# Kernel tuning notes

Hardware: AMD Instinct MI355X
Metric: run time of the kernel (lower is better)

The kernel has to match this reference:

```python
import jax, jax.numpy as jnp
import numpy as np

DIM = 256
HEADS = 8
WS = 16      # window size
WN = 16      # num windows (img 64x64)
KS = 3
B = 16
IMG = 64


def setup_inputs() -> dict:
    key = jax.random.key(0)
    ks = jax.random.split(key, 12)
    d = DIM
    hid = d // 16  # SE hidden (d >= 64)
    inp = {
        "x": jax.random.normal(ks[0], (B, d, IMG, IMG), dtype=jnp.float32),
        "conv_w": jax.random.normal(ks[1], (WN, d, d, KS, KS), dtype=jnp.float32) * 0.02,
        "wqkv": jax.random.normal(ks[2], (d, 3 * d), dtype=jnp.float32) * 0.02,
        "bqkv": jax.random.normal(ks[3], (3 * d,), dtype=jnp.float32) * 0.02,
        "wout": jax.random.normal(ks[4], (d, d), dtype=jnp.float32) * 0.02,
        "bout": jax.random.normal(ks[5], (d,), dtype=jnp.float32) * 0.02,
        "se_w1": jax.random.normal(ks[6], (WN, hid, d), dtype=jnp.float32) * 0.05,
        "se_b1": jax.random.normal(ks[7], (WN, hid), dtype=jnp.float32) * 0.02,
        "se_w2": jax.random.normal(ks[8], (WN, d, hid), dtype=jnp.float32) * 0.05,
        "se_b2": jax.random.normal(ks[9], (WN, d), dtype=jnp.float32) * 0.02,
        "ln_g": jnp.ones((d,), dtype=jnp.float32),
        "ln_b": jnp.zeros((d,), dtype=jnp.float32),
    }
    return inp


def reference(x, conv_w, wqkv, bqkv, wout, bout, se_w1, se_b1, se_w2, se_b2, ln_g, ln_b):
    Bn, C, H, W = x.shape
    hd = C // HEADS
    scale = hd ** (-0.5)

    # window partition: (WN, B, C, WS, WS), windows in (h_idx, w_idx) row-major order
    xw = x.reshape(Bn, C, H // WS, WS, W // WS, WS).transpose(2, 4, 0, 1, 3, 5)
    xw = xw.reshape(WN, Bn, C, WS, WS)

    # kernel tokens: per-layer weight.view(B, C, -1).permute(0,2,1), cat on axis 1
    last = C * KS * KS // Bn
    kt = conv_w.reshape(WN, Bn, C, last).transpose(1, 0, 3, 2).reshape(Bn, WN * last, C)

    # self-attention over kernel tokens (batch axis becomes dim C after reshape)
    qkv = kt @ wqkv + bqkv                                    # (B, WN*last, 3C)
    qkv = qkv.reshape(C, WN * KS * KS, 3, HEADS, hd).transpose(2, 0, 3, 1, 4)
    q, k, v = qkv[0] * scale, qkv[1], qkv[2]                  # (C, H, T, hd), T = WN*KS*KS
    attn = jax.nn.softmax(jnp.einsum('dhqe,dhke->dhqk', q, k), axis=-1)
    o = jnp.einsum('dhqk,dhke->dhqe', attn, v)
    o = o.transpose(0, 2, 1, 3).reshape(C, WN * KS * KS, C)
    o = o @ wout + bout
    kern = o.reshape(C, WN, KS, KS, C).transpose(1, 0, 4, 2, 3)  # (WN, Cout, Cin, KS, KS)

    # SE gating per window: kernels[i] treated as (batch=C, channels=C, KS, KS)
    pooled = kern.mean(axis=(3, 4))                            # (WN, C, C)
    h = jax.nn.relu(jnp.einsum('wbc,whc->wbh', pooled, se_w1) + se_b1[:, None, :])
    s = jax.nn.sigmoid(jnp.einsum('wbh,wch->wbc', h, se_w2) + se_b2[:, None, :])
    kern = kern * s[:, :, :, None, None]

    # per-window conv as a single grouped conv (groups = WN)
    xg = xw.transpose(1, 0, 2, 3, 4).reshape(Bn, WN * C, WS, WS)
    wg = kern.reshape(WN * C, C, KS, KS)
    yg = jax.lax.conv_general_dilated(xg, wg, (1, 1), ((1, 1), (1, 1)),
                                      feature_group_count=WN)
    yw = yg.reshape(Bn, WN, C, WS, WS).transpose(1, 0, 2, 3, 4)  # (WN, B, C, WS, WS)

    # window reverse
    y = yw.reshape(H // WS, W // WS, Bn, C, WS, WS).transpose(2, 3, 0, 4, 1, 5)
    y = y.reshape(Bn, C, H, W)

    # channel layernorm (eps=1e-5) + residual
    yn = y.transpose(0, 2, 3, 1)
    mu = yn.mean(-1, keepdims=True)
    var = ((yn - mu) ** 2).mean(-1, keepdims=True)
    yn = (yn - mu) / jnp.sqrt(var + 1e-5) * ln_g + ln_b
    return x + yn.transpose(0, 3, 1, 2)
```

## Files before the change

kernel.cpp:

```cpp
#include <hip/hip_runtime.h>

typedef __bf16 bf16;
typedef __bf16 bf16x8 __attribute__((ext_vector_type(8)));
typedef _Float16 f16;
typedef _Float16 f16x8 __attribute__((ext_vector_type(8)));
typedef float f32x4 __attribute__((ext_vector_type(4)));

#define SCALE_Q 0.17677669529663687f
#define KSCALE 64.0f
#define KSCALE_INV 0.015625f

__global__ __launch_bounds__(256) void k_prep_w(const float* __restrict__ wqkv,
                                                const float* __restrict__ wout,
                                                bf16* __restrict__ wqkv_t,
                                                f16* __restrict__ wout_h,
                                                f16* __restrict__ wout_l) {
    int n = blockIdx.x, k = threadIdx.x;
    if (n < 768) {
        wqkv_t[n * 256 + k] = (bf16)wqkv[k * 768 + n];
    } else {
        float f = wout[k * 256 + (n - 768)] * KSCALE;
        f16 hi = (f16)f;
        wout_h[(n - 768) * 256 + k] = hi;
        wout_l[(n - 768) * 256 + k] = (f16)(f - (float)hi);
    }
}

__global__ __launch_bounds__(256) void k_build_kt(const float* __restrict__ conv_w,
                                                  bf16* __restrict__ kt) {
    __shared__ float lds[2304];
    int w = blockIdx.x >> 8, co = blockIdx.x & 255;
    const float* src = conv_w + (size_t)(w * 256 + co) * 2304;
    for (int i = threadIdx.x; i < 2304; i += 256) lds[i] = src[i];
    __syncthreads();
    int b = co >> 4, c0 = (co & 15) << 4;
    size_t rbase = (size_t)(b * 16 + w) * 144;
    for (int i = threadIdx.x; i < 2304; i += 256) {
        int t = i >> 4, m = i & 15;
        kt[(rbase + t) * 256 + c0 + m] = (bf16)lds[m * 144 + t];
    }
}

typedef const __attribute__((address_space(1))) unsigned int* gas_t;
typedef __attribute__((address_space(3))) unsigned int* las_t;

__device__ __forceinline__ void async_copy16(const void* g, void* l) {
    __builtin_amdgcn_global_load_lds((gas_t)g, (las_t)l, 16, 0, 0);
}

__device__ __forceinline__ void mfma_tile_bf16(const bf16* As, const bf16* Bs,
                                               f32x4 acc[4][4]) {
    int lane = threadIdx.x & 63;
    int wave = threadIdx.x >> 6;
    int wm = (wave >> 1) * 64, wn = (wave & 1) * 64;
    int lrow = lane & 15, quad = lane >> 4;
    bf16x8 af[4], bfr[4];
#pragma unroll
    for (int i = 0; i < 4; i++) {
        int r = wm + i * 16 + lrow;
        af[i] = *(const bf16x8*)(As + r * 32 + ((quad ^ ((r >> 1) & 3)) << 3));
        int n = wn + i * 16 + lrow;
        bfr[i] = *(const bf16x8*)(Bs + n * 32 + ((quad ^ ((n >> 1) & 3)) << 3));
    }
#pragma unroll
    for (int i = 0; i < 4; i++)
#pragma unroll
        for (int j = 0; j < 4; j++)
            acc[i][j] = __builtin_amdgcn_mfma_f32_16x16x32_bf16(af[i], bfr[j], acc[i][j], 0, 0, 0);
}

__device__ __forceinline__ void mfma_tile_f16_dual(const f16* As, const f16* Bhs,
                                                   const f16* Bls, f32x4 acc[4][4]) {
    int lane = threadIdx.x & 63;
    int wave = threadIdx.x >> 6;
    int wm = (wave >> 1) * 64, wn = (wave & 1) * 64;
    int lrow = lane & 15, quad = lane >> 4;
    f16x8 af[4], bh[4], bl[4];
#pragma unroll
    for (int i = 0; i < 4; i++) {
        int r = wm + i * 16 + lrow;
        af[i] = *(const f16x8*)(As + r * 32 + ((quad ^ ((r >> 1) & 3)) << 3));
        int n = wn + i * 16 + lrow;
        bh[i] = *(const f16x8*)(Bhs + n * 32 + ((quad ^ ((n >> 1) & 3)) << 3));
        bl[i] = *(const f16x8*)(Bls + n * 32 + ((quad ^ ((n >> 1) & 3)) << 3));
    }
#pragma unroll
    for (int i = 0; i < 4; i++)
#pragma unroll
        for (int j = 0; j < 4; j++) {
            acc[i][j] = __builtin_amdgcn_mfma_f32_16x16x32_f16(af[i], bh[j], acc[i][j], 0, 0, 0);
            acc[i][j] = __builtin_amdgcn_mfma_f32_16x16x32_f16(af[i], bl[j], acc[i][j], 0, 0, 0);
        }
}

__device__ __forceinline__ void mfma_tile_f16_dual8(const f16* As, const f16* Bhs,
                                                    const f16* Bls, f32x4 acc[8][4]) {
    int lane = threadIdx.x & 63;
    int wave = threadIdx.x >> 6;
    int wm = (wave >> 1) * 128, wn = (wave & 1) * 64;
    int lrow = lane & 15, quad = lane >> 4;
    f16x8 af[8], bh[4], bl[4];
#pragma unroll
    for (int i = 0; i < 8; i++) {
        int r = wm + i * 16 + lrow;
        af[i] = *(const f16x8*)(As + r * 32 + ((quad ^ ((r >> 1) & 3)) << 3));
    }
#pragma unroll
    for (int j = 0; j < 4; j++) {
        int n = wn + j * 16 + lrow;
        bh[j] = *(const f16x8*)(Bhs + n * 32 + ((quad ^ ((n >> 1) & 3)) << 3));
        bl[j] = *(const f16x8*)(Bls + n * 32 + ((quad ^ ((n >> 1) & 3)) << 3));
    }
#pragma unroll
    for (int i = 0; i < 8; i++)
#pragma unroll
        for (int j = 0; j < 4; j++) {
            acc[i][j] = __builtin_amdgcn_mfma_f32_16x16x32_f16(af[i], bh[j], acc[i][j], 0, 0, 0);
            acc[i][j] = __builtin_amdgcn_mfma_f32_16x16x32_f16(af[i], bl[j], acc[i][j], 0, 0, 0);
        }
}

__global__ __launch_bounds__(256) void k_gemm_qkv(const bf16* __restrict__ A,
                                                  const bf16* __restrict__ Bt,
                                                  const float* __restrict__ bias,
                                                  bf16* __restrict__ outb,
                                                  int N, int K) {
    __shared__ __align__(16) bf16 As[2][128 * 32];
    __shared__ __align__(16) bf16 Bs[2][128 * 32];
    int m0 = blockIdx.y * 128, n0 = blockIdx.x * 128;
    int t = threadIdx.x, wave = t >> 6, lane = t & 63;
    int chunk0 = wave * 2, chunk1 = chunk0 + 1;
    int row0 = chunk0 * 16 + (lane >> 2), row1 = row0 + 16;
    int sw = ((lane & 3) ^ ((row0 >> 1) & 3)) << 3;
    const unsigned short* Ag = (const unsigned short*)A;
    const unsigned short* Bg = (const unsigned short*)Bt;
    size_t a0 = (size_t)(m0 + row0) * K + sw, a1 = (size_t)(m0 + row1) * K + sw;
    size_t b0 = (size_t)(n0 + row0) * K + sw, b1 = (size_t)(n0 + row1) * K + sw;
    f32x4 acc[4][4] = {};
#define STG_QKV(cur, k0)                                        \
    async_copy16(Ag + a0 + (k0), &As[cur][chunk0 * 512]);       \
    async_copy16(Ag + a1 + (k0), &As[cur][chunk1 * 512]);       \
    async_copy16(Bg + b0 + (k0), &Bs[cur][chunk0 * 512]);       \
    async_copy16(Bg + b1 + (k0), &Bs[cur][chunk1 * 512]);
    STG_QKV(0, 0);
    int cur = 0, NT = K >> 5;
#pragma unroll 1
    for (int it = 0; it < NT; it++) {
        if (it < NT - 1) {
            STG_QKV(cur ^ 1, (it + 1) << 5);
            asm volatile("s_waitcnt vmcnt(4)" ::: "memory");
        } else {
            asm volatile("s_waitcnt vmcnt(0)" ::: "memory");
        }
        __builtin_amdgcn_s_barrier();
        mfma_tile_bf16(As[cur], Bs[cur], acc);
        asm volatile("s_waitcnt lgkmcnt(0)" ::: "memory");
        __builtin_amdgcn_s_barrier();
        cur ^= 1;
    }
#undef STG_QKV
    int wm = (wave >> 1) * 64, wn = (wave & 1) * 64;
    int lrow = lane & 15, quad = lane >> 4;
#pragma unroll
    for (int i = 0; i < 4; i++)
#pragma unroll
        for (int j = 0; j < 4; j++) {
            int col = n0 + wn + j * 16 + lrow;
            float bv = bias[col];
#pragma unroll
            for (int rr = 0; rr < 4; rr++) {
                int row = m0 + wm + i * 16 + quad * 4 + rr;
                float v = acc[i][j][rr] + bv;
                if (col < 256) v *= SCALE_Q;
                outb[(size_t)row * N + col] = (bf16)v;
            }
        }
}

__global__ __launch_bounds__(256) void k_gemm_split2(const f16* __restrict__ Ag_,
                                                     const f16* __restrict__ Bhg,
                                                     const f16* __restrict__ Blg,
                                                     const float* __restrict__ bias,
                                                     float* __restrict__ outf,
                                                     int N, int K) {
    __shared__ __align__(16) f16 As[2][128 * 32];
    __shared__ __align__(16) f16 Bh[2][128 * 32];
    __shared__ __align__(16) f16 Bl[2][128 * 32];
    int m0 = blockIdx.y * 128, n0 = blockIdx.x * 128;
    int t = threadIdx.x, wave = t >> 6, lane = t & 63;
    int chunk0 = wave * 2, chunk1 = chunk0 + 1;
    int row0 = chunk0 * 16 + (lane >> 2), row1 = row0 + 16;
    int sw = ((lane & 3) ^ ((row0 >> 1) & 3)) << 3;
    const unsigned short* Au = (const unsigned short*)Ag_;
    const unsigned short* Bhu = (const unsigned short*)Bhg;
    const unsigned short* Blu = (const unsigned short*)Blg;
    size_t a0 = (size_t)(m0 + row0) * K + sw, a1 = (size_t)(m0 + row1) * K + sw;
    size_t b0 = (size_t)(n0 + row0) * K + sw, b1 = (size_t)(n0 + row1) * K + sw;
    f32x4 acc[4][4] = {};
#define STG_SP2(cur, k0)                                        \
    async_copy16(Au + a0 + (k0), &As[cur][chunk0 * 512]);       \
    async_copy16(Au + a1 + (k0), &As[cur][chunk1 * 512]);       \
    async_copy16(Bhu + b0 + (k0), &Bh[cur][chunk0 * 512]);      \
    async_copy16(Bhu + b1 + (k0), &Bh[cur][chunk1 * 512]);      \
    async_copy16(Blu + b0 + (k0), &Bl[cur][chunk0 * 512]);      \
    async_copy16(Blu + b1 + (k0), &Bl[cur][chunk1 * 512]);
    STG_SP2(0, 0);
    int cur = 0, NT = K >> 5;
#pragma unroll 1
    for (int it = 0; it < NT; it++) {
        if (it < NT - 1) {
            STG_SP2(cur ^ 1, (it + 1) << 5);
            asm volatile("s_waitcnt vmcnt(6)" ::: "memory");
        } else {
            asm volatile("s_waitcnt vmcnt(0)" ::: "memory");
        }
        __builtin_amdgcn_s_barrier();
        mfma_tile_f16_dual(As[cur], Bh[cur], Bl[cur], acc);
        asm volatile("s_waitcnt lgkmcnt(0)" ::: "memory");
        __builtin_amdgcn_s_barrier();
        cur ^= 1;
    }
#undef STG_SP2
    int wm = (wave >> 1) * 64, wn = (wave & 1) * 64;
    int lrow = lane & 15, quad = lane >> 4;
#pragma unroll
    for (int i = 0; i < 4; i++)
#pragma unroll
        for (int j = 0; j < 4; j++) {
            int col = n0 + wn + j * 16 + lrow;
            float bv = bias[col];
#pragma unroll
            for (int rr = 0; rr < 4; rr++) {
                int row = m0 + wm + i * 16 + quad * 4 + rr;
                outf[(size_t)row * N + col] = acc[i][j][rr] * KSCALE_INV + bv;
            }
        }
}

__global__ __launch_bounds__(256) void k_attn(const bf16* __restrict__ qkv,
                                              f16* __restrict__ o16) {
    __shared__ bf16 Qs[144 * 32];
    __shared__ bf16 Ks[144 * 32];
    __shared__ f16 Vt[32 * 160];
    __shared__ f16 Ps[4 * 16 * 168];
    int d = blockIdx.x >> 3, h = blockIdx.x & 7;
    const bf16* base = qkv + (size_t)d * 144 * 768 + h * 32;
    int t = threadIdx.x;

    for (int i = t; i < 512; i += 256) Vt[(i >> 4) * 160 + 144 + (i & 15)] = (f16)0.f;
    for (int i = t; i < 576; i += 256) {
        int row = i >> 2, part = i & 3;
        const bf16* rp = base + (size_t)row * 768;
        uint4 vq = *(const uint4*)(rp + (part << 3));
        uint4 vk = *(const uint4*)(rp + 256 + (part << 3));
        int sw = ((part ^ (row & 3)) << 3);
        *(uint4*)(Qs + row * 32 + sw) = vq;
        *(uint4*)(Ks + row * 32 + sw) = vk;
        bf16x8 v8 = *(const bf16x8*)(rp + 512 + (part << 3));
#pragma unroll
        for (int j = 0; j < 8; j++) Vt[(part * 8 + j) * 160 + row] = (f16)(float)v8[j];
    }
    __syncthreads();

    int wave = t >> 6, lane = t & 63;
    int lrow = lane & 15, quad = lane >> 4;
    f16* Pw = Ps + wave * 16 * 168;
    for (int i = lane; i < 256; i += 64) Pw[(i >> 4) * 168 + 144 + (i & 15)] = (f16)0.f;

    bf16x8 kf[9];
#pragma unroll
    for (int nt = 0; nt < 9; nt++) {
        int r = nt * 16 + lrow;
        kf[nt] = *(const bf16x8*)(Ks + r * 32 + ((quad ^ (r & 3)) << 3));
    }

    for (int mt = wave; mt < 9; mt += 4) {
        int qr = mt * 16 + lrow;
        bf16x8 qf = *(const bf16x8*)(Qs + qr * 32 + ((quad ^ (qr & 3)) << 3));
        f32x4 s[9];
#pragma unroll
        for (int nt = 0; nt < 9; nt++) {
            f32x4 z = {0.f, 0.f, 0.f, 0.f};
            s[nt] = __builtin_amdgcn_mfma_f32_16x16x32_bf16(qf, kf[nt], z, 0, 0, 0);
        }
        f32x4 mx = s[0];
#pragma unroll
        for (int nt = 1; nt < 9; nt++)
#pragma unroll
            for (int c = 0; c < 4; c++) mx[c] = fmaxf(mx[c], s[nt][c]);
#pragma unroll
        for (int off = 1; off < 16; off <<= 1)
#pragma unroll
            for (int c = 0; c < 4; c++) mx[c] = fmaxf(mx[c], __shfl_xor(mx[c], off));
        f32x4 sm = {0.f, 0.f, 0.f, 0.f};
#pragma unroll
        for (int nt = 0; nt < 9; nt++)
#pragma unroll
            for (int c = 0; c < 4; c++) {
                float e = __expf(s[nt][c] - mx[c]);
                s[nt][c] = e;
                sm[c] += e;
            }
#pragma unroll
        for (int off = 1; off < 16; off <<= 1)
#pragma unroll
            for (int c = 0; c < 4; c++) sm[c] += __shfl_xor(sm[c], off);
        f32x4 inv;
#pragma unroll
        for (int c = 0; c < 4; c++) inv[c] = 1.f / sm[c];
#pragma unroll
        for (int nt = 0; nt < 9; nt++)
#pragma unroll
            for (int c = 0; c < 4; c++)
                Pw[(quad * 4 + c) * 168 + nt * 16 + lrow] = (f16)(s[nt][c] * inv[c]);

        f32x4 o0 = {0.f, 0.f, 0.f, 0.f}, o1 = {0.f, 0.f, 0.f, 0.f};
#pragma unroll
        for (int kt = 0; kt < 5; kt++) {
            f16x8 pf = *(const f16x8*)(Pw + lrow * 168 + kt * 32 + quad * 8);
            f16x8 v0 = *(const f16x8*)(Vt + lrow * 160 + kt * 32 + quad * 8);
            f16x8 v1 = *(const f16x8*)(Vt + (16 + lrow) * 160 + kt * 32 + quad * 8);
            o0 = __builtin_amdgcn_mfma_f32_16x16x32_f16(pf, v0, o0, 0, 0, 0);
            o1 = __builtin_amdgcn_mfma_f32_16x16x32_f16(pf, v1, o1, 0, 0, 0);
        }
        size_t ro = ((size_t)d * 144 + mt * 16) * 256 + h * 32;
#pragma unroll
        for (int c = 0; c < 4; c++) {
            size_t rr = ro + (size_t)(quad * 4 + c) * 256;
            o16[rr + lrow] = (f16)o0[c];
            o16[rr + 16 + lrow] = (f16)o1[c];
        }
    }
}

__global__ __launch_bounds__(256) void k_se_scale(const float* __restrict__ kern,
                                                  const float* __restrict__ w1,
                                                  const float* __restrict__ b1,
                                                  const float* __restrict__ w2,
                                                  const float* __restrict__ b2,
                                                  f16* __restrict__ kern_hi,
                                                  f16* __restrict__ kern_lo) {
    __shared__ float pooled[256];
    __shared__ float hbuf[16];
    int w = blockIdx.x >> 8, Co = blockIdx.x & 255;
    int ci = threadIdx.x;
    const float* kb = kern + (size_t)(Co * 16 + w) * 9 * 256;
    float pv = 0.f;
#pragma unroll
    for (int k9 = 0; k9 < 9; k9++) pv += kb[k9 * 256 + ci];
    pooled[ci] = pv * (1.f / 9.f);
    __syncthreads();
    if (ci < 16) {
        const float* w1p = w1 + (size_t)(w * 16 + ci) * 256;
        float hs = b1[w * 16 + ci];
        for (int c = 0; c < 256; c++) hs += pooled[c] * w1p[c];
        hbuf[ci] = fmaxf(hs, 0.f);
    }
    __syncthreads();
    const float* w2p = w2 + (size_t)(w * 256 + ci) * 16;
    float ss = b2[w * 256 + ci];
#pragma unroll
    for (int j = 0; j < 16; j++) ss += hbuf[j] * w2p[j];
    float s = (1.f / (1.f + __expf(-ss))) * KSCALE;
    size_t outo = (size_t)(w * 256 + Co) * 2304;
    f16* khi = kern_hi + outo;
    f16* klo = kern_lo + outo;
#pragma unroll
    for (int k9 = 0; k9 < 9; k9++) {
        float f = kb[k9 * 256 + ci] * s;
        f16 hi = (f16)f;
        khi[k9 * 256 + ci] = hi;
        klo[k9 * 256 + ci] = (f16)(f - (float)hi);
    }
}

__global__ __launch_bounds__(256) void k_zero(uint4* __restrict__ p, int n4) {
    int stride = gridDim.x * 256;
    for (int i = blockIdx.x * 256 + threadIdx.x; i < n4; i += stride)
        p[i] = uint4{0u, 0u, 0u, 0u};
}

__global__ __launch_bounds__(256) void k_fill_xcl(const float* __restrict__ x,
                                                  f16* __restrict__ xcl) {
    int bx = blockIdx.x;
    int b = bx >> 6, gy = bx & 63;
    int wrow = gy >> 4, py = gy & 15;
    int ci = threadIdx.x;
    const float* xp = x + ((size_t)(b * 256 + ci) * 64 + gy) * 64;
    for (int wx = 0; wx < 4; wx++) {
        int w = wrow * 4 + wx;
        size_t o = (((size_t)(w * 16 + b) * 18 + py + 1) * 18 + 1) * 256 + ci;
#pragma unroll
        for (int px = 0; px < 16; px++)
            xcl[o + (size_t)px * 256] = (f16)xp[wx * 16 + px];
    }
}

__global__ __launch_bounds__(256, 2) void k_conv_gemm(const f16* __restrict__ xcl,
                                                      const f16* __restrict__ kern_hi,
                                                      const f16* __restrict__ kern_lo,
                                                      float* __restrict__ y) {
    __shared__ __align__(16) f16 As[2][256 * 32];
    __shared__ __align__(16) f16 Bh[2][128 * 32];
    __shared__ __align__(16) f16 Bl[2][128 * 32];
    int w = blockIdx.z;
    int m0 = blockIdx.y * 256, n0 = blockIdx.x * 128;
    const unsigned short* xw = (const unsigned short*)(xcl + (size_t)w * 16 * 18 * 18 * 256);
    const unsigned short* Bthu = (const unsigned short*)(kern_hi + (size_t)w * 256 * 2304);
    const unsigned short* Btlu = (const unsigned short*)(kern_lo + (size_t)w * 256 * 2304);
    int t = threadIdx.x, wave = t >> 6, lane = t & 63;
    int sw = ((lane & 3) ^ ((lane >> 3) & 3)) << 3;
    size_t aA[4];
#pragma unroll
    for (int c = 0; c < 4; c++) {
        int row = (wave * 4 + c) * 16 + (lane >> 2);
        int py = row >> 4, px = row & 15;
        aA[c] = ((size_t)(blockIdx.y * 18 + py) * 18 + px) * 256 + sw;
    }
    int rb0 = (wave * 2) * 16 + (lane >> 2), rb1 = rb0 + 16;
    size_t bB0 = (size_t)(n0 + rb0) * 2304 + sw;
    size_t bB1 = (size_t)(n0 + rb1) * 2304 + sw;
    f32x4 acc[8][4] = {};
#define STG_CONV(cur, k0)                                                      \
    {                                                                          \
        int k9_ = (k0) >> 8;                                                   \
        int koff_ = ((k9_ / 3) * 18 + (k9_ % 3)) * 256 + ((k0) & 255);         \
        async_copy16(xw + aA[0] + koff_, &As[cur][(wave * 4 + 0) * 512]);      \
        async_copy16(xw + aA[1] + koff_, &As[cur][(wave * 4 + 1) * 512]);      \
        async_copy16(xw + aA[2] + koff_, &As[cur][(wave * 4 + 2) * 512]);      \
        async_copy16(xw + aA[3] + koff_, &As[cur][(wave * 4 + 3) * 512]);      \
        async_copy16(Bthu + bB0 + (k0), &Bh[cur][(wave * 2 + 0) * 512]);       \
        async_copy16(Bthu + bB1 + (k0), &Bh[cur][(wave * 2 + 1) * 512]);       \
        async_copy16(Btlu + bB0 + (k0), &Bl[cur][(wave * 2 + 0) * 512]);       \
        async_copy16(Btlu + bB1 + (k0), &Bl[cur][(wave * 2 + 1) * 512]);       \
    }
    STG_CONV(0, 0);
    int cur = 0;
#pragma unroll 1
    for (int it = 0; it < 72; it++) {
        if (it < 71) {
            STG_CONV(cur ^ 1, (it + 1) << 5);
            asm volatile("s_waitcnt vmcnt(8)" ::: "memory");
        } else {
            asm volatile("s_waitcnt vmcnt(0)" ::: "memory");
        }
        __builtin_amdgcn_s_barrier();
        mfma_tile_f16_dual8(As[cur], Bh[cur], Bl[cur], acc);
        asm volatile("s_waitcnt lgkmcnt(0)" ::: "memory");
        __builtin_amdgcn_s_barrier();
        cur ^= 1;
    }
#undef STG_CONV
    int lrow = lane & 15, quad = lane >> 4;
    int wm = (wave >> 1) * 128, wn = (wave & 1) * 64;
    float* yw = y + (size_t)w * 4096 * 256;
#pragma unroll
    for (int i = 0; i < 8; i++)
#pragma unroll
        for (int j = 0; j < 4; j++) {
            int col = n0 + wn + j * 16 + lrow;
#pragma unroll
            for (int rr = 0; rr < 4; rr++) {
                int row = m0 + wm + i * 16 + quad * 4 + rr;
                yw[(size_t)row * 256 + col] = acc[i][j][rr] * KSCALE_INV;
            }
        }
}

__global__ __launch_bounds__(256) void k_ln_res(const float* __restrict__ y,
                                                const float* __restrict__ x,
                                                const float* __restrict__ g,
                                                const float* __restrict__ be,
                                                float* __restrict__ out) {
    int bx = blockIdx.x;
    int b = bx >> 6, gy = bx & 63;
    int t = threadIdx.x;
    int j = t >> 2, sub = t & 3;
    int w = (gy >> 4) * 4 + (j >> 4);
    int p = (gy & 15) * 16 + (j & 15);
    const float* yp = y + ((size_t)w * 4096 + b * 256 + p) * 256 + sub * 64;
    float vals[64];
    float sum = 0.f, sq = 0.f;
#pragma unroll
    for (int c = 0; c < 64; c++) {
        float v = yp[c];
        vals[c] = v;
        sum += v; sq += v * v;
    }
    sum += __shfl_xor(sum, 1); sq += __shfl_xor(sq, 1);
    sum += __shfl_xor(sum, 2); sq += __shfl_xor(sq, 2);
    float mean = sum * (1.f / 256.f);
    float var = sq * (1.f / 256.f) - mean * mean;
    float rstd = rsqrtf(var + 1e-5f);
    const float* xp = x + ((size_t)(b * 256 + sub * 64) * 64 + gy) * 64 + j;
    float* op = out + ((size_t)(b * 256 + sub * 64) * 64 + gy) * 64 + j;
#pragma unroll
    for (int c = 0; c < 64; c++) {
        int cc = sub * 64 + c;
        op[(size_t)c * 4096] = (vals[c] - mean) * rstd * g[cc] + be[cc] + xp[(size_t)c * 4096];
    }
}

extern "C" void kernel_launch(void* const* d_in, const int* in_sizes, int n_in,
                              void* d_out, int out_size, void* d_ws, size_t ws_size,
                              hipStream_t stream) {
    const float* x      = (const float*)d_in[0];
    const float* conv_w = (const float*)d_in[1];
    const float* wqkv   = (const float*)d_in[2];
    const float* bqkv   = (const float*)d_in[3];
    const float* wout   = (const float*)d_in[4];
    const float* bout   = (const float*)d_in[5];
    const float* se_w1  = (const float*)d_in[6];
    const float* se_b1  = (const float*)d_in[7];
    const float* se_w2  = (const float*)d_in[8];
    const float* se_b2  = (const float*)d_in[9];
    const float* ln_g   = (const float*)d_in[10];
    const float* ln_b   = (const float*)d_in[11];
    float* out = (float*)d_out;

    char* ws = (char*)d_ws;
    bf16*  kt      = (bf16*)(ws + 0);
    f16*   o16     = (f16*)(ws + 0);
    f16*   kern_hi = (f16*)(ws + 0);
    f16*   kern_lo = (f16*)(ws + 18874368);
    bf16*  wqkv_t  = (bf16*)(ws + 37748736);
    f16*   wout_h  = (f16*)(ws + 38141952);
    f16*   wout_l  = (f16*)(ws + 38273024);
    f16*   xcl     = (f16*)(ws + 38404096);
    bf16*  qkv     = (bf16*)(ws + 80871424);
    float* kern_f  = (float*)(ws + 80871424);
    float* y       = (float*)(ws + 80871424);

    k_prep_w<<<1024, 256, 0, stream>>>(wqkv, wout, wqkv_t, wout_h, wout_l);
    k_build_kt<<<4096, 256, 0, stream>>>(conv_w, kt);
    k_gemm_qkv<<<dim3(6, 288), 256, 0, stream>>>(kt, wqkv_t, bqkv, qkv, 768, 256);
    k_attn<<<2048, 256, 0, stream>>>(qkv, o16);
    k_gemm_split2<<<dim3(2, 288), 256, 0, stream>>>(o16, wout_h, wout_l, bout, kern_f, 256, 256);
    k_se_scale<<<4096, 256, 0, stream>>>(kern_f, se_w1, se_b1, se_w2, se_b2, kern_hi, kern_lo);
    k_zero<<<2048, 256, 0, stream>>>((uint4*)xcl, 42467328 / 16);
    k_fill_xcl<<<1024, 256, 0, stream>>>(x, xcl);
    k_conv_gemm<<<dim3(2, 16, 16), 256, 0, stream>>>(xcl, kern_hi, kern_lo, y);
    k_ln_res<<<1024, 256, 0, stream>>>(y, x, ln_g, ln_b, out);
}
```

Before: 510.9 us.

## Remap conv GEMM blocks per XCD and parallelize SE hidden reduction

The conv GEMM grid is flattened to 1D, and block indices are remapped so that each of the 8 XCDs handles two whole windows. This is meant to keep each window's weight and input tiles within one XCD's L2. In k_se_scale, the 16-thread serial dot product for the SE hidden layer becomes a 256-thread strided sum with a shuffle reduction. The kernel values are also kept in registers so they are not reloaded from global memory. The remap assumes round-robin dispatch of blocks to XCDs.

```diff
diff --git a/kernel.cpp b/kernel.cpp
--- a/kernel.cpp
+++ b/kernel.cpp
@@ -345,16 +345,23 @@
     int w = blockIdx.x >> 8, Co = blockIdx.x & 255;
     int ci = threadIdx.x;
     const float* kb = kern + (size_t)(Co * 16 + w) * 9 * 256;
+    float v9[9];
     float pv = 0.f;
 #pragma unroll
-    for (int k9 = 0; k9 < 9; k9++) pv += kb[k9 * 256 + ci];
+    for (int k9 = 0; k9 < 9; k9++) { v9[k9] = kb[k9 * 256 + ci]; pv += v9[k9]; }
     pooled[ci] = pv * (1.f / 9.f);
     __syncthreads();
-    if (ci < 16) {
-        const float* w1p = w1 + (size_t)(w * 16 + ci) * 256;
-        float hs = b1[w * 16 + ci];
-        for (int c = 0; c < 256; c++) hs += pooled[c] * w1p[c];
-        hbuf[ci] = fmaxf(hs, 0.f);
+    {
+        int hid = ci >> 4, l16 = ci & 15;
+        const float* w1p = w1 + (size_t)(w * 16 + hid) * 256;
+        float hs = 0.f;
+#pragma unroll
+        for (int c = l16; c < 256; c += 16) hs += pooled[c] * w1p[c];
+        hs += __shfl_xor(hs, 1);
+        hs += __shfl_xor(hs, 2);
+        hs += __shfl_xor(hs, 4);
+        hs += __shfl_xor(hs, 8);
+        if (l16 == 0) hbuf[hid] = fmaxf(hs + b1[w * 16 + hid], 0.f);
     }
     __syncthreads();
     const float* w2p = w2 + (size_t)(w * 256 + ci) * 16;
@@ -367,7 +374,7 @@
     f16* klo = kern_lo + outo;
 #pragma unroll
     for (int k9 = 0; k9 < 9; k9++) {
-        float f = kb[k9 * 256 + ci] * s;
+        float f = v9[k9] * s;
         f16 hi = (f16)f;
         khi[k9 * 256 + ci] = hi;
         klo[k9 * 256 + ci] = (f16)(f - (float)hi);
@@ -403,8 +410,13 @@
     __shared__ __align__(16) f16 As[2][256 * 32];
     __shared__ __align__(16) f16 Bh[2][128 * 32];
     __shared__ __align__(16) f16 Bl[2][128 * 32];
-    int w = blockIdx.z;
-    int m0 = blockIdx.y * 256, n0 = blockIdx.x * 128;
+    int f = blockIdx.x;
+    int xcd = f & 7, i5 = f >> 3;
+    int w = xcd * 2 + (i5 >> 5);
+    int rem = i5 & 31;
+    int by = rem >> 1;
+    int n0 = (rem & 1) * 128;
+    int m0 = by * 256;
     const unsigned short* xw = (const unsigned short*)(xcl + (size_t)w * 16 * 18 * 18 * 256);
     const unsigned short* Bthu = (const unsigned short*)(kern_hi + (size_t)w * 256 * 2304);
     const unsigned short* Btlu = (const unsigned short*)(kern_lo + (size_t)w * 256 * 2304);
@@ -415,7 +427,7 @@
     for (int c = 0; c < 4; c++) {
         int row = (wave * 4 + c) * 16 + (lane >> 2);
         int py = row >> 4, px = row & 15;
-        aA[c] = ((size_t)(blockIdx.y * 18 + py) * 18 + px) * 256 + sw;
+        aA[c] = ((size_t)(by * 18 + py) * 18 + px) * 256 + sw;
     }
     int rb0 = (wave * 2) * 16 + (lane >> 2), rb1 = rb0 + 16;
     size_t bB0 = (size_t)(n0 + rb0) * 2304 + sw;
@@ -539,6 +551,6 @@
     k_se_scale<<<4096, 256, 0, stream>>>(kern_f, se_w1, se_b1, se_w2, se_b2, kern_hi, kern_lo);
     k_zero<<<2048, 256, 0, stream>>>((uint4*)xcl, 42467328 / 16);
     k_fill_xcl<<<1024, 256, 0, stream>>>(x, xcl);
-    k_conv_gemm<<<dim3(2, 16, 16), 256, 0, stream>>>(xcl, kern_hi, kern_lo, y);
+    k_conv_gemm<<<512, 256, 0, stream>>>(xcl, kern_hi, kern_lo, y);
     k_ln_res<<<1024, 256, 0, stream>>>(y, x, ln_g, ln_b, out);
 }
```

Measured after the change: 480.4 us. 1.06x faster.
